# Performance work log

Hardware: AMD Instinct MI355X
Metric: run time of the kernel (lower is better)

The kernel has to match this reference:

```python
import jax, jax.numpy as jnp
import numpy as np
import math

B, S, D, H = 1, 4096, 1024, 16
HD = D // H  # head_dim = 64


def setup_inputs() -> dict:
    key = jax.random.key(0)
    ks = jax.random.split(key, 6)
    x = jax.random.normal(ks[0], (B, S, D), dtype=jnp.float32)
    # Llama-style rotary frequencies: theta = 10000^{-2i/head_dim}
    inv_freq = 1.0 / (10000.0 ** (jnp.arange(0, HD, 2, dtype=jnp.float32) / HD))  # (HD/2,)
    t = jnp.arange(S, dtype=jnp.float32)
    freqs = jnp.outer(t, inv_freq)  # (S, HD/2)
    cos = jnp.cos(freqs)
    sin = jnp.sin(freqs)
    # additive causal mask (S, S): 0 on/below diagonal, -inf above
    mask = jnp.where(jnp.tril(jnp.ones((S, S), dtype=bool)), 0.0, -jnp.inf).astype(jnp.float32)
    scale = 1.0 / math.sqrt(D)
    wq = jax.random.normal(ks[1], (D, D), dtype=jnp.float32) * scale
    wk = jax.random.normal(ks[2], (D, D), dtype=jnp.float32) * scale
    wv = jax.random.normal(ks[3], (D, D), dtype=jnp.float32) * scale
    wo = jax.random.normal(ks[4], (D, D), dtype=jnp.float32) * scale
    return {"x": x, "cos": cos, "sin": sin, "mask": mask,
            "wq": wq, "wk": wk, "wv": wv, "wo": wo, "start_pos": 0}


def _rope(t, cos, sin):
    # t: (b, s, h, hd); cos/sin: (s, hd/2). Interleaved-pair complex rotation.
    b, s, h, hd = t.shape
    tr = t.reshape(b, s, h, hd // 2, 2)
    te, to = tr[..., 0], tr[..., 1]
    c = cos[None, :, None, :]
    sn = sin[None, :, None, :]
    oe = te * c - to * sn
    oo = te * sn + to * c
    return jnp.stack([oe, oo], axis=-1).reshape(b, s, h, hd)


def reference(x, cos, sin, mask, wq, wk, wv, wo, start_pos):
    b, s, d = x.shape
    h, hd = H, HD
    # Linear layers: y = x @ W.T (torch nn.Linear convention, W is (out,in))
    xq = (x @ wq.T).reshape(b, s, h, hd)
    xk = (x @ wk.T).reshape(b, s, h, hd)
    xv = (x @ wv.T).reshape(b, s, h, hd)
    xq = _rope(xq, cos, sin)
    xk = _rope(xk, cos, sin)
    # (b, h, s, hd)
    xq = xq.transpose(0, 2, 1, 3)
    xk = xk.transpose(0, 2, 1, 3)
    xv = xv.transpose(0, 2, 1, 3)
    scores = jnp.einsum('bhqd,bhkd->bhqk', xq, xk) / math.sqrt(hd)
    scores = scores + mask[None, None, :, :]
    attn = jax.nn.softmax(scores.astype(jnp.float32), axis=-1).astype(xq.dtype)
    out = jnp.einsum('bhqk,bhkd->bhqd', attn, xv)
    out = out.transpose(0, 2, 1, 3).reshape(b, s, d)
    return out @ wo.T
```

## Files before the change

kernel.cpp:

```cpp
#include <hip/hip_runtime.h>
#include <hip/hip_bf16.h>
#include <math.h>

typedef __bf16 bf16;
typedef __bf16 bf16x4 __attribute__((ext_vector_type(4)));
typedef __bf16 bf16x8 __attribute__((ext_vector_type(8)));
typedef float floatx4 __attribute__((ext_vector_type(4)));
typedef short short4v __attribute__((ext_vector_type(4)));

#define S_LEN 4096
#define DM 1024
#define NH 16
#define HD 64

#define GM 4096
#define GN 1024
#define GK 1024
#define FST 68

#define GLDS16(gp, lp) __builtin_amdgcn_global_load_lds( \
    (const __attribute__((address_space(1))) void*)(gp), \
    (__attribute__((address_space(3))) void*)(lp), 16, 0, 0)

__global__ void cvt_bf16(const float* __restrict__ x,  const float* __restrict__ wq,
                         const float* __restrict__ wk, const float* __restrict__ wv,
                         const float* __restrict__ wo, bf16* __restrict__ dst)
{
    size_t i4 = ((size_t)blockIdx.x * 256 + threadIdx.x) * 4;
    const float* src; size_t off;
    const size_t M1 = (size_t)1 << 20;
    if      (i4 < 4 * M1) { src = x;  off = i4;          }
    else if (i4 < 5 * M1) { src = wq; off = i4 - 4 * M1; }
    else if (i4 < 6 * M1) { src = wk; off = i4 - 5 * M1; }
    else if (i4 < 7 * M1) { src = wv; off = i4 - 6 * M1; }
    else                  { src = wo; off = i4 - 7 * M1; }
    float4 v = *(const float4*)(src + off);
    bf16x4 o = { (bf16)v.x, (bf16)v.y, (bf16)v.z, (bf16)v.w };
    *(bf16x4*)(&dst[i4]) = o;
}

__launch_bounds__(256)
__global__ void gemm_qkv(const bf16* __restrict__ A,
                         const bf16* __restrict__ B0, const bf16* __restrict__ B1,
                         const bf16* __restrict__ B2,
                         const float* __restrict__ cosp, const float* __restrict__ sinp,
                         bf16* __restrict__ Qw, bf16* __restrict__ Kw,
                         bf16* __restrict__ VTw)
{
    const int bz = blockIdx.z;
    const bf16* __restrict__ B = (bz == 0) ? B0 : (bz == 1 ? B1 : B2);

    const int tid  = threadIdx.x;
    const int wave = tid >> 6;
    const int lane = tid & 63;
    const int wm   = (wave >> 1) * 32;
    const int wn   = (wave & 1) * 64;
    const int lrow = lane >> 4;
    const int lcol = lane & 15;

    const int m0 = blockIdx.y * 64;
    const int n0 = blockIdx.x * 128;

    __shared__ __align__(16) bf16 As[64 * 64];
    __shared__ __align__(16) bf16 Bs[128 * 64];

    floatx4 acc[2][4];
    #pragma unroll
    for (int i = 0; i < 2; i++)
        #pragma unroll
        for (int j = 0; j < 4; j++) acc[i][j] = (floatx4){0.f, 0.f, 0.f, 0.f};

    const bf16* ga0 = A + (size_t)(m0 + wave * 16 + (lane >> 3)) * GK + (lane & 7) * 8;
    const bf16* gb0 = B + (size_t)(n0 + wave * 32 + (lane >> 3)) * GK + (lane & 7) * 8;
    bf16* la = &As[(wave * 16) * 64];
    bf16* lb = &Bs[(wave * 32) * 64];

    for (int kt = 0; kt < GK; kt += 64) {
        #pragma unroll
        for (int i = 0; i < 2; i++)
            GLDS16(ga0 + kt + (size_t)i * 8 * GK, la + i * 8 * 64);
        #pragma unroll
        for (int i = 0; i < 4; i++)
            GLDS16(gb0 + kt + (size_t)i * 8 * GK, lb + i * 8 * 64);
        __syncthreads();
        #pragma unroll
        for (int ks = 0; ks < 2; ks++) {
            bf16x8 af[2], bfr[4];
            #pragma unroll
            for (int t = 0; t < 2; t++)
                af[t]  = *(const bf16x8*)(&As[(wm + t * 16 + lcol) * 64 + ks * 32 + lrow * 8]);
            #pragma unroll
            for (int t = 0; t < 4; t++)
                bfr[t] = *(const bf16x8*)(&Bs[(wn + t * 16 + lcol) * 64 + ks * 32 + lrow * 8]);
            #pragma unroll
            for (int mt = 0; mt < 2; mt++)
                #pragma unroll
                for (int nt = 0; nt < 4; nt++)
                    acc[mt][nt] = __builtin_amdgcn_mfma_f32_16x16x32_bf16(af[mt], bfr[nt], acc[mt][nt], 0, 0, 0);
        }
        __syncthreads();
    }

    if (bz < 2) {
        bf16* __restrict__ C = bz ? Kw : Qw;
        const bool odd = (lcol & 1);
        #pragma unroll
        for (int mt = 0; mt < 2; mt++)
            #pragma unroll
            for (int nt = 0; nt < 4; nt++) {
                int i = (nt * 16 + lcol) >> 1;
                #pragma unroll
                for (int r = 0; r < 4; r++) {
                    float v  = acc[mt][nt][r];
                    float pv = __shfl_xor(v, 1, 64);
                    int s = m0 + wm + mt * 16 + lrow * 4 + r;
                    float c  = cosp[s * 32 + i];
                    float sn = sinp[s * 32 + i];
                    float ov = odd ? (pv * sn + v * c) : (v * c - pv * sn);
                    C[(size_t)s * GN + n0 + wn + nt * 16 + lcol] = (bf16)ov;
                }
            }
    } else {
        #pragma unroll
        for (int mt = 0; mt < 2; mt++)
            #pragma unroll
            for (int nt = 0; nt < 4; nt++) {
                int col = n0 + wn + nt * 16 + lcol;
                int s   = m0 + wm + mt * 16 + lrow * 4;
                bf16x4 ov = { (bf16)acc[mt][nt][0], (bf16)acc[mt][nt][1],
                              (bf16)acc[mt][nt][2], (bf16)acc[mt][nt][3] };
                *(bf16x4*)(&VTw[(size_t)col * S_LEN + s]) = ov;
            }
    }
}

__launch_bounds__(256, 4)
__global__ void flash_attn(const bf16* __restrict__ Q, const bf16* __restrict__ K,
                           const bf16* __restrict__ VT,
                           float* __restrict__ O0, float* __restrict__ O1,
                           float* __restrict__ L0, float* __restrict__ L1)
{
    const int pi   = blockIdx.x >> 1;
    const int p    = blockIdx.x & 1;
    const int h    = blockIdx.y;
    const int tid  = threadIdx.x;
    const int wave = tid >> 6;
    const int lane = tid & 63;
    const int lrow = lane >> 4;
    const int lcol = lane & 15;

    const int qtA = pi;
    const int qtB = 63 - pi;

    float* __restrict__ Op = p ? O1 : O0;
    float* __restrict__ Lp = p ? L1 : L0;

    __shared__ __align__(16) bf16 Ks[2][64 * FST];
    __shared__ __align__(16) bf16 Vs[2][64 * FST];

    const float sc2 = 0.125f * 1.44269504088896340736f;

    const int q0A = qtA * 64 + wave * 16;
    const int q0B = qtB * 64 + wave * 16;

    const bf16* qpA = Q + (size_t)(q0A + lcol) * DM + h * HD;
    const bf16* qpB = Q + (size_t)(q0B + lcol) * DM + h * HD;
    bf16x8 qfA[2], qfB[2];
    qfA[0] = *(const bf16x8*)(qpA + 0 + lrow * 8);
    qfA[1] = *(const bf16x8*)(qpA + 32 + lrow * 8);
    qfB[0] = *(const bf16x8*)(qpB + 0 + lrow * 8);
    qfB[1] = *(const bf16x8*)(qpB + 32 + lrow * 8);

    float lA = 0.f, lB = 0.f;
    floatx4 oaccA[4], oaccB[4];
    #pragma unroll
    for (int nt = 0; nt < 4; nt++) {
        oaccA[nt] = (floatx4){0.f, 0.f, 0.f, 0.f};
        oaccB[nt] = (floatx4){0.f, 0.f, 0.f, 0.f};
    }

    const int  srow = tid >> 3;
    const int  sch  = (tid & 7) * 8;
    const bf16* kp  = K  + (size_t)srow * DM + h * HD + sch;
    const bf16* vp  = VT + (size_t)(h * HD + srow) * S_LEN + sch;
    const int  wof  = srow * FST + sch;

    {
        size_t ko = (size_t)p * 64 * DM;
        size_t vo = (size_t)p * 64;
        uint4 a = *(const uint4*)(kp + ko);
        uint4 b = *(const uint4*)(kp + ko + (size_t)32 * DM);
        uint4 c = *(const uint4*)(vp + vo);
        uint4 d = *(const uint4*)(vp + vo + (size_t)32 * S_LEN);
        *(uint4*)(&Ks[0][wof])            = a;
        *(uint4*)(&Ks[0][wof + 32 * FST]) = b;
        *(uint4*)(&Vs[0][wof])            = c;
        *(uint4*)(&Vs[0][wof + 32 * FST]) = d;
    }
    __syncthreads();

    uint4 kr0, kr1, vr0, vr1;
    for (int t = p; t <= qtB; t += 2) {
        const int  cur  = ((t - p) >> 1) & 1;
        const bool more = (t + 2 <= qtB);
        const bool actA = (t <= qtA);

        if (more) {
            size_t ko = (size_t)(t + 2) * 64 * DM;
            size_t vo = (size_t)(t + 2) * 64;
            kr0 = *(const uint4*)(kp + ko);
            kr1 = *(const uint4*)(kp + ko + (size_t)32 * DM);
            vr0 = *(const uint4*)(vp + vo);
            vr1 = *(const uint4*)(vp + vo + (size_t)32 * S_LEN);
        }

        short4v pbA[4], pbB[4];
        const bool diagA = (t == qtA);
        const bool diagB = (t == qtB);
        #pragma unroll
        for (int nt = 0; nt < 4; nt++) {
            floatx4 zB = (floatx4){0.f, 0.f, 0.f, 0.f};
            floatx4 zA = (floatx4){0.f, 0.f, 0.f, 0.f};
            #pragma unroll
            for (int ks = 0; ks < 2; ks++) {
                bf16x8 kf = *(const bf16x8*)(&Ks[cur][(nt * 16 + lcol) * FST + ks * 32 + lrow * 8]);
                zB = __builtin_amdgcn_mfma_f32_16x16x32_bf16(kf, qfB[ks], zB, 0, 0, 0);
                if (actA)
                    zA = __builtin_amdgcn_mfma_f32_16x16x32_bf16(kf, qfA[ks], zA, 0, 0, 0);
            }
            if (diagB) {
                #pragma unroll
                for (int r = 0; r < 4; r++) {
                    int kg = t * 64 + nt * 16 + lrow * 4 + r;
                    float pr = exp2f(zB[r] * sc2);
                    if (kg > q0B + lcol) pr = 0.f;
                    zB[r] = pr; lB += pr;
                }
            } else {
                #pragma unroll
                for (int r = 0; r < 4; r++) {
                    float pr = exp2f(zB[r] * sc2);
                    zB[r] = pr; lB += pr;
                }
            }
            bf16x4 pvB = { (bf16)zB[0], (bf16)zB[1], (bf16)zB[2], (bf16)zB[3] };
            pbB[nt] = __builtin_bit_cast(short4v, pvB);
            if (actA) {
                if (diagA) {
                    #pragma unroll
                    for (int r = 0; r < 4; r++) {
                        int kg = t * 64 + nt * 16 + lrow * 4 + r;
                        float pr = exp2f(zA[r] * sc2);
                        if (kg > q0A + lcol) pr = 0.f;
                        zA[r] = pr; lA += pr;
                    }
                } else {
                    #pragma unroll
                    for (int r = 0; r < 4; r++) {
                        float pr = exp2f(zA[r] * sc2);
                        zA[r] = pr; lA += pr;
                    }
                }
                bf16x4 pvA = { (bf16)zA[0], (bf16)zA[1], (bf16)zA[2], (bf16)zA[3] };
                pbA[nt] = __builtin_bit_cast(short4v, pvA);
            }
        }

        #pragma unroll
        for (int nt = 0; nt < 4; nt++)
            #pragma unroll
            for (int kt = 0; kt < 4; kt++) {
                bf16x4 va = *(const bf16x4*)(&Vs[cur][(nt * 16 + lcol) * FST + kt * 16 + lrow * 4]);
                short4v vas = __builtin_bit_cast(short4v, va);
                oaccB[nt] = __builtin_amdgcn_mfma_f32_16x16x16bf16_1k(vas, pbB[kt], oaccB[nt], 0, 0, 0);
                if (actA)
                    oaccA[nt] = __builtin_amdgcn_mfma_f32_16x16x16bf16_1k(vas, pbA[kt], oaccA[nt], 0, 0, 0);
            }

        if (more) {
            int nxt = cur ^ 1;
            *(uint4*)(&Ks[nxt][wof])            = kr0;
            *(uint4*)(&Ks[nxt][wof + 32 * FST]) = kr1;
            *(uint4*)(&Vs[nxt][wof])            = vr0;
            *(uint4*)(&Vs[nxt][wof + 32 * FST]) = vr1;
        }
        __syncthreads();
    }

    lA += __shfl_xor(lA, 16, 64);
    lA += __shfl_xor(lA, 32, 64);
    lB += __shfl_xor(lB, 16, 64);
    lB += __shfl_xor(lB, 32, 64);
    if (lrow == 0) {
        Lp[h * S_LEN + q0A + lcol] = lA;
        Lp[h * S_LEN + q0B + lcol] = lB;
    }
    #pragma unroll
    for (int nt = 0; nt < 4; nt++) {
        *(floatx4*)(&Op[(size_t)(q0A + lcol) * DM + h * HD + nt * 16 + lrow * 4]) = oaccA[nt];
        *(floatx4*)(&Op[(size_t)(q0B + lcol) * DM + h * HD + nt * 16 + lrow * 4]) = oaccB[nt];
    }
}

__global__ void combine_kernel(const float* __restrict__ O0, const float* __restrict__ O1,
                               const float* __restrict__ L0, const float* __restrict__ L1,
                               bf16* __restrict__ Aw)
{
    int i4 = (blockIdx.x * 256 + threadIdx.x) * 4;
    int q = i4 >> 10;
    int c = i4 & 1023;
    int h = c >> 6;
    float rl = 1.f / (L0[h * S_LEN + q] + L1[h * S_LEN + q]);
    float4 a = *(const float4*)(O0 + i4);
    float4 b = *(const float4*)(O1 + i4);
    bf16x4 o = { (bf16)((a.x + b.x) * rl), (bf16)((a.y + b.y) * rl),
                 (bf16)((a.z + b.z) * rl), (bf16)((a.w + b.w) * rl) };
    *(bf16x4*)(&Aw[i4]) = o;
}

__launch_bounds__(256)
__global__ void gemm_out(const bf16* __restrict__ A, const bf16* __restrict__ B,
                         float* __restrict__ out)
{
    const int tid  = threadIdx.x;
    const int wave = tid >> 6;
    const int lane = tid & 63;
    const int wm   = (wave >> 1) * 32;
    const int wn   = (wave & 1) * 64;
    const int lrow = lane >> 4;
    const int lcol = lane & 15;

    const int m0 = blockIdx.y * 64;
    const int n0 = blockIdx.x * 128;

    __shared__ __align__(16) bf16 As[64 * 64];
    __shared__ __align__(16) bf16 Bs[128 * 64];

    floatx4 acc[2][4];
    #pragma unroll
    for (int i = 0; i < 2; i++)
        #pragma unroll
        for (int j = 0; j < 4; j++) acc[i][j] = (floatx4){0.f, 0.f, 0.f, 0.f};

    const bf16* ga0 = A + (size_t)(m0 + wave * 16 + (lane >> 3)) * GK + (lane & 7) * 8;
    const bf16* gb0 = B + (size_t)(n0 + wave * 32 + (lane >> 3)) * GK + (lane & 7) * 8;
    bf16* la = &As[(wave * 16) * 64];
    bf16* lb = &Bs[(wave * 32) * 64];

    for (int kt = 0; kt < GK; kt += 64) {
        #pragma unroll
        for (int i = 0; i < 2; i++)
            GLDS16(ga0 + kt + (size_t)i * 8 * GK, la + i * 8 * 64);
        #pragma unroll
        for (int i = 0; i < 4; i++)
            GLDS16(gb0 + kt + (size_t)i * 8 * GK, lb + i * 8 * 64);
        __syncthreads();
        #pragma unroll
        for (int ks = 0; ks < 2; ks++) {
            bf16x8 af[2], bfr[4];
            #pragma unroll
            for (int t = 0; t < 2; t++)
                af[t]  = *(const bf16x8*)(&As[(wm + t * 16 + lcol) * 64 + ks * 32 + lrow * 8]);
            #pragma unroll
            for (int t = 0; t < 4; t++)
                bfr[t] = *(const bf16x8*)(&Bs[(wn + t * 16 + lcol) * 64 + ks * 32 + lrow * 8]);
            #pragma unroll
            for (int mt = 0; mt < 2; mt++)
                #pragma unroll
                for (int nt = 0; nt < 4; nt++)
                    acc[mt][nt] = __builtin_amdgcn_mfma_f32_16x16x32_bf16(af[mt], bfr[nt], acc[mt][nt], 0, 0, 0);
        }
        __syncthreads();
    }

    #pragma unroll
    for (int mt = 0; mt < 2; mt++)
        #pragma unroll
        for (int nt = 0; nt < 4; nt++)
            #pragma unroll
            for (int r = 0; r < 4; r++) {
                int row = m0 + wm + mt * 16 + lrow * 4 + r;
                int col = n0 + wn + nt * 16 + lcol;
                out[(size_t)row * GN + col] = acc[mt][nt][r];
            }
}

extern "C" void kernel_launch(void* const* d_in, const int* in_sizes, int n_in,
                              void* d_out, int out_size, void* d_ws, size_t ws_size,
                              hipStream_t stream) {
    const float* x    = (const float*)d_in[0];
    const float* cosp = (const float*)d_in[1];
    const float* sinp = (const float*)d_in[2];
    const float* wq   = (const float*)d_in[4];
    const float* wk   = (const float*)d_in[5];
    const float* wv   = (const float*)d_in[6];
    const float* wo   = (const float*)d_in[7];
    float* out = (float*)d_out;

    const size_t SD = (size_t)S_LEN * DM;
    const size_t DD = (size_t)DM * DM;
    bf16* xb  = (bf16*)d_ws;
    bf16* wqb = xb + SD;
    bf16* wkb = wqb + DD;
    bf16* wvb = wkb + DD;
    bf16* wob = wvb + DD;
    bf16* Qw  = wob + DD;
    bf16* Kw  = Qw + SD;
    bf16* VTw = Kw + SD;
    bf16* Aw  = VTw + SD;
    float* O0f = (float*)(Aw + SD);
    float* O1f = O0f + SD;
    float* L0f = O1f + SD;
    float* L1f = L0f + (size_t)S_LEN * NH;

    cvt_bf16<<<8192, 256, 0, stream>>>(x, wq, wk, wv, wo, xb);
    gemm_qkv<<<dim3(GN / 128, GM / 64, 3), 256, 0, stream>>>(
        xb, wqb, wkb, wvb, cosp, sinp, Qw, Kw, VTw);
    flash_attn<<<dim3(64, NH), 256, 0, stream>>>(Qw, Kw, VTw, O0f, O1f, L0f, L1f);
    combine_kernel<<<S_LEN * DM / 1024, 256, 0, stream>>>(O0f, O1f, L0f, L1f, Aw);
    gemm_out<<<dim3(GN / 128, GM / 64), 256, 0, stream>>>(Aw, wob, out);
}
```

Baseline: 286.9 us.

## Split attention KV range three ways, swizzle LDS tiles, add MFMA priority hints

The flash attention kernel is templated on the number of KV-range splits. It now uses three partial passes when the workspace is large enough, with a three-way combine kernel, so more blocks can fill the GPU. The padded LDS layout is replaced by an XOR-swizzled 64-wide layout, which shrinks shared memory and avoids bank conflicts. Launch bounds rise to 5 blocks per CU, s_setprio brackets the MFMA sections, and the row-sum is accumulated per register component. The cost is an extra partial-output buffer to read and write, plus possible register pressure at the higher occupancy target.

```diff
diff --git a/kernel.cpp b/kernel.cpp
--- a/kernel.cpp
+++ b/kernel.cpp
@@ -16,7 +16,6 @@
 #define GM 4096
 #define GN 1024
 #define GK 1024
-#define FST 68
 
 #define GLDS16(gp, lp) __builtin_amdgcn_global_load_lds( \
     (const __attribute__((address_space(1))) void*)(gp), \
@@ -134,29 +133,35 @@
     }
 }
 
-__launch_bounds__(256, 4)
+#define KSW(row, chunk) (((row) << 6) + ((((chunk) ^ ((row) & 7))) << 3))
+
+template<int STEP>
+__launch_bounds__(256, 5)
 __global__ void flash_attn(const bf16* __restrict__ Q, const bf16* __restrict__ K,
                            const bf16* __restrict__ VT,
                            float* __restrict__ O0, float* __restrict__ O1,
-                           float* __restrict__ L0, float* __restrict__ L1)
-{
-    const int pi   = blockIdx.x >> 1;
-    const int p    = blockIdx.x & 1;
+                           float* __restrict__ O2,
+                           float* __restrict__ L0, float* __restrict__ L1,
+                           float* __restrict__ L2)
+{
+    const int pi   = blockIdx.x / STEP;
+    const int p    = blockIdx.x % STEP;
     const int h    = blockIdx.y;
     const int tid  = threadIdx.x;
     const int wave = tid >> 6;
     const int lane = tid & 63;
     const int lrow = lane >> 4;
     const int lcol = lane & 15;
+    const int rsw  = lcol & 7;
 
     const int qtA = pi;
     const int qtB = 63 - pi;
 
-    float* __restrict__ Op = p ? O1 : O0;
-    float* __restrict__ Lp = p ? L1 : L0;
-
-    __shared__ __align__(16) bf16 Ks[2][64 * FST];
-    __shared__ __align__(16) bf16 Vs[2][64 * FST];
+    float* __restrict__ Op = (p == 0) ? O0 : (p == 1 ? O1 : O2);
+    float* __restrict__ Lp = (p == 0) ? L0 : (p == 1 ? L1 : L2);
+
+    __shared__ __align__(16) bf16 Ks[2][64 * 64];
+    __shared__ __align__(16) bf16 Vs[2][64 * 64];
 
     const float sc2 = 0.125f * 1.44269504088896340736f;
 
@@ -171,7 +176,8 @@
     qfB[0] = *(const bf16x8*)(qpB + 0 + lrow * 8);
     qfB[1] = *(const bf16x8*)(qpB + 32 + lrow * 8);
 
-    float lA = 0.f, lB = 0.f;
+    floatx4 lA4 = (floatx4){0.f, 0.f, 0.f, 0.f};
+    floatx4 lB4 = (floatx4){0.f, 0.f, 0.f, 0.f};
     floatx4 oaccA[4], oaccB[4];
     #pragma unroll
     for (int nt = 0; nt < 4; nt++) {
@@ -180,10 +186,10 @@
     }
 
     const int  srow = tid >> 3;
-    const int  sch  = (tid & 7) * 8;
-    const bf16* kp  = K  + (size_t)srow * DM + h * HD + sch;
-    const bf16* vp  = VT + (size_t)(h * HD + srow) * S_LEN + sch;
-    const int  wof  = srow * FST + sch;
+    const int  schk = tid & 7;
+    const bf16* kp  = K  + (size_t)srow * DM + h * HD + schk * 8;
+    const bf16* vp  = VT + (size_t)(h * HD + srow) * S_LEN + schk * 8;
+    const int  wof  = KSW(srow, schk);
 
     {
         size_t ko = (size_t)p * 64 * DM;
@@ -192,22 +198,22 @@
         uint4 b = *(const uint4*)(kp + ko + (size_t)32 * DM);
         uint4 c = *(const uint4*)(vp + vo);
         uint4 d = *(const uint4*)(vp + vo + (size_t)32 * S_LEN);
-        *(uint4*)(&Ks[0][wof])            = a;
-        *(uint4*)(&Ks[0][wof + 32 * FST]) = b;
-        *(uint4*)(&Vs[0][wof])            = c;
-        *(uint4*)(&Vs[0][wof + 32 * FST]) = d;
+        *(uint4*)(&Ks[0][wof])           = a;
+        *(uint4*)(&Ks[0][wof + 32 * 64]) = b;
+        *(uint4*)(&Vs[0][wof])           = c;
+        *(uint4*)(&Vs[0][wof + 32 * 64]) = d;
     }
     __syncthreads();
 
     uint4 kr0, kr1, vr0, vr1;
-    for (int t = p; t <= qtB; t += 2) {
-        const int  cur  = ((t - p) >> 1) & 1;
-        const bool more = (t + 2 <= qtB);
+    for (int t = p; t <= qtB; t += STEP) {
+        const int  cur  = ((t - p) / STEP) & 1;
+        const bool more = (t + STEP <= qtB);
         const bool actA = (t <= qtA);
 
         if (more) {
-            size_t ko = (size_t)(t + 2) * 64 * DM;
-            size_t vo = (size_t)(t + 2) * 64;
+            size_t ko = (size_t)(t + STEP) * 64 * DM;
+            size_t vo = (size_t)(t + STEP) * 64;
             kr0 = *(const uint4*)(kp + ko);
             kr1 = *(const uint4*)(kp + ko + (size_t)32 * DM);
             vr0 = *(const uint4*)(vp + vo);
@@ -221,26 +227,29 @@
         for (int nt = 0; nt < 4; nt++) {
             floatx4 zB = (floatx4){0.f, 0.f, 0.f, 0.f};
             floatx4 zA = (floatx4){0.f, 0.f, 0.f, 0.f};
+            __builtin_amdgcn_s_setprio(1);
             #pragma unroll
             for (int ks = 0; ks < 2; ks++) {
-                bf16x8 kf = *(const bf16x8*)(&Ks[cur][(nt * 16 + lcol) * FST + ks * 32 + lrow * 8]);
+                bf16x8 kf = *(const bf16x8*)(&Ks[cur][((nt * 16 + lcol) << 6) +
+                                             ((((ks << 2) + lrow) ^ rsw) << 3)]);
                 zB = __builtin_amdgcn_mfma_f32_16x16x32_bf16(kf, qfB[ks], zB, 0, 0, 0);
                 if (actA)
                     zA = __builtin_amdgcn_mfma_f32_16x16x32_bf16(kf, qfA[ks], zA, 0, 0, 0);
             }
+            __builtin_amdgcn_s_setprio(0);
             if (diagB) {
                 #pragma unroll
                 for (int r = 0; r < 4; r++) {
                     int kg = t * 64 + nt * 16 + lrow * 4 + r;
                     float pr = exp2f(zB[r] * sc2);
                     if (kg > q0B + lcol) pr = 0.f;
-                    zB[r] = pr; lB += pr;
+                    zB[r] = pr; lB4[r] += pr;
                 }
             } else {
                 #pragma unroll
                 for (int r = 0; r < 4; r++) {
                     float pr = exp2f(zB[r] * sc2);
-                    zB[r] = pr; lB += pr;
+                    zB[r] = pr; lB4[r] += pr;
                 }
             }
             bf16x4 pvB = { (bf16)zB[0], (bf16)zB[1], (bf16)zB[2], (bf16)zB[3] };
@@ -252,13 +261,13 @@
                         int kg = t * 64 + nt * 16 + lrow * 4 + r;
                         float pr = exp2f(zA[r] * sc2);
                         if (kg > q0A + lcol) pr = 0.f;
-                        zA[r] = pr; lA += pr;
+                        zA[r] = pr; lA4[r] += pr;
                     }
                 } else {
                     #pragma unroll
                     for (int r = 0; r < 4; r++) {
                         float pr = exp2f(zA[r] * sc2);
-                        zA[r] = pr; lA += pr;
+                        zA[r] = pr; lA4[r] += pr;
                     }
                 }
                 bf16x4 pvA = { (bf16)zA[0], (bf16)zA[1], (bf16)zA[2], (bf16)zA[3] };
@@ -266,27 +275,32 @@
             }
         }
 
+        __builtin_amdgcn_s_setprio(1);
         #pragma unroll
         for (int nt = 0; nt < 4; nt++)
             #pragma unroll
             for (int kt = 0; kt < 4; kt++) {
-                bf16x4 va = *(const bf16x4*)(&Vs[cur][(nt * 16 + lcol) * FST + kt * 16 + lrow * 4]);
+                bf16x4 va = *(const bf16x4*)(&Vs[cur][((nt * 16 + lcol) << 6) +
+                              ((((kt << 1) + (lrow >> 1)) ^ rsw) << 3) + ((lrow & 1) << 2)]);
                 short4v vas = __builtin_bit_cast(short4v, va);
                 oaccB[nt] = __builtin_amdgcn_mfma_f32_16x16x16bf16_1k(vas, pbB[kt], oaccB[nt], 0, 0, 0);
                 if (actA)
                     oaccA[nt] = __builtin_amdgcn_mfma_f32_16x16x16bf16_1k(vas, pbA[kt], oaccA[nt], 0, 0, 0);
             }
+        __builtin_amdgcn_s_setprio(0);
 
         if (more) {
             int nxt = cur ^ 1;
-            *(uint4*)(&Ks[nxt][wof])            = kr0;
-            *(uint4*)(&Ks[nxt][wof + 32 * FST]) = kr1;
-            *(uint4*)(&Vs[nxt][wof])            = vr0;
-            *(uint4*)(&Vs[nxt][wof + 32 * FST]) = vr1;
+            *(uint4*)(&Ks[nxt][wof])           = kr0;
+            *(uint4*)(&Ks[nxt][wof + 32 * 64]) = kr1;
+            *(uint4*)(&Vs[nxt][wof])           = vr0;
+            *(uint4*)(&Vs[nxt][wof + 32 * 64]) = vr1;
         }
         __syncthreads();
     }
 
+    float lA = lA4[0] + lA4[1] + lA4[2] + lA4[3];
+    float lB = lB4[0] + lB4[1] + lB4[2] + lB4[3];
     lA += __shfl_xor(lA, 16, 64);
     lA += __shfl_xor(lA, 32, 64);
     lB += __shfl_xor(lB, 16, 64);
@@ -302,9 +316,9 @@
     }
 }
 
-__global__ void combine_kernel(const float* __restrict__ O0, const float* __restrict__ O1,
-                               const float* __restrict__ L0, const float* __restrict__ L1,
-                               bf16* __restrict__ Aw)
+__global__ void combine2(const float* __restrict__ O0, const float* __restrict__ O1,
+                         const float* __restrict__ L0, const float* __restrict__ L1,
+                         bf16* __restrict__ Aw)
 {
     int i4 = (blockIdx.x * 256 + threadIdx.x) * 4;
     int q = i4 >> 10;
@@ -315,6 +329,25 @@
     float4 b = *(const float4*)(O1 + i4);
     bf16x4 o = { (bf16)((a.x + b.x) * rl), (bf16)((a.y + b.y) * rl),
                  (bf16)((a.z + b.z) * rl), (bf16)((a.w + b.w) * rl) };
+    *(bf16x4*)(&Aw[i4]) = o;
+}
+
+__global__ void combine3(const float* __restrict__ O0, const float* __restrict__ O1,
+                         const float* __restrict__ O2,
+                         const float* __restrict__ L0, const float* __restrict__ L1,
+                         const float* __restrict__ L2,
+                         bf16* __restrict__ Aw)
+{
+    int i4 = (blockIdx.x * 256 + threadIdx.x) * 4;
+    int q = i4 >> 10;
+    int c = i4 & 1023;
+    int h = c >> 6;
+    float rl = 1.f / (L0[h * S_LEN + q] + L1[h * S_LEN + q] + L2[h * S_LEN + q]);
+    float4 a = *(const float4*)(O0 + i4);
+    float4 b = *(const float4*)(O1 + i4);
+    float4 cc = *(const float4*)(O2 + i4);
+    bf16x4 o = { (bf16)((a.x + b.x + cc.x) * rl), (bf16)((a.y + b.y + cc.y) * rl),
+                 (bf16)((a.z + b.z + cc.z) * rl), (bf16)((a.w + b.w + cc.w) * rl) };
     *(bf16x4*)(&Aw[i4]) = o;
 }
 
@@ -412,11 +445,23 @@
     float* O1f = O0f + SD;
     float* L0f = O1f + SD;
     float* L1f = L0f + (size_t)S_LEN * NH;
+    float* O2f = L1f + (size_t)S_LEN * NH;
+    float* L2f = O2f + SD;
+    size_t need3 = (size_t)((char*)(L2f + (size_t)S_LEN * NH) - (char*)d_ws);
 
     cvt_bf16<<<8192, 256, 0, stream>>>(x, wq, wk, wv, wo, xb);
     gemm_qkv<<<dim3(GN / 128, GM / 64, 3), 256, 0, stream>>>(
         xb, wqb, wkb, wvb, cosp, sinp, Qw, Kw, VTw);
-    flash_attn<<<dim3(64, NH), 256, 0, stream>>>(Qw, Kw, VTw, O0f, O1f, L0f, L1f);
-    combine_kernel<<<S_LEN * DM / 1024, 256, 0, stream>>>(O0f, O1f, L0f, L1f, Aw);
+    if (ws_size >= need3) {
+        flash_attn<3><<<dim3(96, NH), 256, 0, stream>>>(
+            Qw, Kw, VTw, O0f, O1f, O2f, L0f, L1f, L2f);
+        combine3<<<S_LEN * DM / 1024, 256, 0, stream>>>(
+            O0f, O1f, O2f, L0f, L1f, L2f, Aw);
+    } else {
+        flash_attn<2><<<dim3(64, NH), 256, 0, stream>>>(
+            Qw, Kw, VTw, O0f, O1f, O0f, L0f, L1f, L0f);
+        combine2<<<S_LEN * DM / 1024, 256, 0, stream>>>(
+            O0f, O1f, L0f, L1f, Aw);
+    }
     gemm_out<<<dim3(GN / 128, GM / 64), 256, 0, stream>>>(Aw, wob, out);
 }
```

New measurement: 473.5 us. +65.1%, slower.

## Double-buffer and swizzle GEMM LDS tiles, fold softmax scale into Q, MFMA row sums

Applied to the files above, without the earlier changes.

Both GEMM kernels now keep two LDS buffers and prefetch the next K-tile while the current one is being computed. They also XOR-swizzle the 16-byte chunks in LDS to cut bank conflicts on the fragment reads. The attention scale times log2(e) is folded into Q in the projection epilogue, which removes a multiply per score in the softmax. The per-row softmax denominator is now accumulated with an MFMA against a ones vector instead of scalar adds and cross-lane shuffles. The costs are double the LDS per GEMM block, which can lower occupancy, and slightly different rounding because Q is scaled before the bf16 cast.

```diff
diff --git a/kernel.cpp b/kernel.cpp
--- a/kernel.cpp
+++ b/kernel.cpp
@@ -17,6 +17,8 @@
 #define GN 1024
 #define GK 1024
 #define FST 68
+
+#define QSCALE 0.18033688011112042f
 
 #define GLDS16(gp, lp) __builtin_amdgcn_global_load_lds( \
     (const __attribute__((address_space(1))) void*)(gp), \
@@ -61,8 +63,8 @@
     const int m0 = blockIdx.y * 64;
     const int n0 = blockIdx.x * 128;
 
-    __shared__ __align__(16) bf16 As[64 * 64];
-    __shared__ __align__(16) bf16 Bs[128 * 64];
+    __shared__ __align__(16) bf16 As[2][64 * 64];
+    __shared__ __align__(16) bf16 Bs[2][128 * 64];
 
     floatx4 acc[2][4];
     #pragma unroll
@@ -70,28 +72,40 @@
         #pragma unroll
         for (int j = 0; j < 4; j++) acc[i][j] = (floatx4){0.f, 0.f, 0.f, 0.f};
 
-    const bf16* ga0 = A + (size_t)(m0 + wave * 16 + (lane >> 3)) * GK + (lane & 7) * 8;
-    const bf16* gb0 = B + (size_t)(n0 + wave * 32 + (lane >> 3)) * GK + (lane & 7) * 8;
-    bf16* la = &As[(wave * 16) * 64];
-    bf16* lb = &Bs[(wave * 32) * 64];
-
+    const int swc = (((lane & 7) ^ ((lane >> 3) & 7))) * 8;
+    const bf16* ga0 = A + (size_t)(m0 + wave * 16 + (lane >> 3)) * GK + swc;
+    const bf16* gb0 = B + (size_t)(n0 + wave * 32 + (lane >> 3)) * GK + swc;
+    const int kof0 = ((0 + lrow) ^ (lcol & 7)) * 8;
+    const int kof1 = ((4 + lrow) ^ (lcol & 7)) * 8;
+
+    #pragma unroll
+    for (int i = 0; i < 2; i++)
+        GLDS16(ga0 + (size_t)i * 8 * GK, &As[0][(wave * 16 + i * 8) * 64]);
+    #pragma unroll
+    for (int i = 0; i < 4; i++)
+        GLDS16(gb0 + (size_t)i * 8 * GK, &Bs[0][(wave * 32 + i * 8) * 64]);
+    __syncthreads();
+
+    int cur = 0;
     for (int kt = 0; kt < GK; kt += 64) {
-        #pragma unroll
-        for (int i = 0; i < 2; i++)
-            GLDS16(ga0 + kt + (size_t)i * 8 * GK, la + i * 8 * 64);
-        #pragma unroll
-        for (int i = 0; i < 4; i++)
-            GLDS16(gb0 + kt + (size_t)i * 8 * GK, lb + i * 8 * 64);
-        __syncthreads();
+        if (kt + 64 < GK) {
+            #pragma unroll
+            for (int i = 0; i < 2; i++)
+                GLDS16(ga0 + kt + 64 + (size_t)i * 8 * GK, &As[cur ^ 1][(wave * 16 + i * 8) * 64]);
+            #pragma unroll
+            for (int i = 0; i < 4; i++)
+                GLDS16(gb0 + kt + 64 + (size_t)i * 8 * GK, &Bs[cur ^ 1][(wave * 32 + i * 8) * 64]);
+        }
         #pragma unroll
         for (int ks = 0; ks < 2; ks++) {
+            const int ko = ks ? kof1 : kof0;
             bf16x8 af[2], bfr[4];
             #pragma unroll
             for (int t = 0; t < 2; t++)
-                af[t]  = *(const bf16x8*)(&As[(wm + t * 16 + lcol) * 64 + ks * 32 + lrow * 8]);
+                af[t]  = *(const bf16x8*)(&As[cur][(wm + t * 16 + lcol) * 64 + ko]);
             #pragma unroll
             for (int t = 0; t < 4; t++)
-                bfr[t] = *(const bf16x8*)(&Bs[(wn + t * 16 + lcol) * 64 + ks * 32 + lrow * 8]);
+                bfr[t] = *(const bf16x8*)(&Bs[cur][(wn + t * 16 + lcol) * 64 + ko]);
             #pragma unroll
             for (int mt = 0; mt < 2; mt++)
                 #pragma unroll
@@ -99,10 +113,12 @@
                     acc[mt][nt] = __builtin_amdgcn_mfma_f32_16x16x32_bf16(af[mt], bfr[nt], acc[mt][nt], 0, 0, 0);
         }
         __syncthreads();
+        cur ^= 1;
     }
 
     if (bz < 2) {
         bf16* __restrict__ C = bz ? Kw : Qw;
+        const float qs = (bz == 0) ? QSCALE : 1.0f;
         const bool odd = (lcol & 1);
         #pragma unroll
         for (int mt = 0; mt < 2; mt++)
@@ -117,7 +133,7 @@
                     float c  = cosp[s * 32 + i];
                     float sn = sinp[s * 32 + i];
                     float ov = odd ? (pv * sn + v * c) : (v * c - pv * sn);
-                    C[(size_t)s * GN + n0 + wn + nt * 16 + lcol] = (bf16)ov;
+                    C[(size_t)s * GN + n0 + wn + nt * 16 + lcol] = (bf16)(ov * qs);
                 }
             }
     } else {
@@ -158,8 +174,6 @@
     __shared__ __align__(16) bf16 Ks[2][64 * FST];
     __shared__ __align__(16) bf16 Vs[2][64 * FST];
 
-    const float sc2 = 0.125f * 1.44269504088896340736f;
-
     const int q0A = qtA * 64 + wave * 16;
     const int q0B = qtB * 64 + wave * 16;
 
@@ -171,7 +185,12 @@
     qfB[0] = *(const bf16x8*)(qpB + 0 + lrow * 8);
     qfB[1] = *(const bf16x8*)(qpB + 32 + lrow * 8);
 
-    float lA = 0.f, lB = 0.f;
+    const bf16 one_b = (bf16)1.0f;
+    const bf16x4 onev = { one_b, one_b, one_b, one_b };
+    const short4v ones_s = __builtin_bit_cast(short4v, onev);
+
+    floatx4 laccA = (floatx4){0.f, 0.f, 0.f, 0.f};
+    floatx4 laccB = (floatx4){0.f, 0.f, 0.f, 0.f};
     floatx4 oaccA[4], oaccB[4];
     #pragma unroll
     for (int nt = 0; nt < 4; nt++) {
@@ -232,16 +251,14 @@
                 #pragma unroll
                 for (int r = 0; r < 4; r++) {
                     int kg = t * 64 + nt * 16 + lrow * 4 + r;
-                    float pr = exp2f(zB[r] * sc2);
+                    float pr = exp2f(zB[r]);
                     if (kg > q0B + lcol) pr = 0.f;
-                    zB[r] = pr; lB += pr;
+                    zB[r] = pr;
                 }
             } else {
                 #pragma unroll
-                for (int r = 0; r < 4; r++) {
-                    float pr = exp2f(zB[r] * sc2);
-                    zB[r] = pr; lB += pr;
-                }
+                for (int r = 0; r < 4; r++)
+                    zB[r] = exp2f(zB[r]);
             }
             bf16x4 pvB = { (bf16)zB[0], (bf16)zB[1], (bf16)zB[2], (bf16)zB[3] };
             pbB[nt] = __builtin_bit_cast(short4v, pvB);
@@ -250,20 +267,25 @@
                     #pragma unroll
                     for (int r = 0; r < 4; r++) {
                         int kg = t * 64 + nt * 16 + lrow * 4 + r;
-                        float pr = exp2f(zA[r] * sc2);
+                        float pr = exp2f(zA[r]);
                         if (kg > q0A + lcol) pr = 0.f;
-                        zA[r] = pr; lA += pr;
+                        zA[r] = pr;
                     }
                 } else {
                     #pragma unroll
-                    for (int r = 0; r < 4; r++) {
-                        float pr = exp2f(zA[r] * sc2);
-                        zA[r] = pr; lA += pr;
-                    }
+                    for (int r = 0; r < 4; r++)
+                        zA[r] = exp2f(zA[r]);
                 }
                 bf16x4 pvA = { (bf16)zA[0], (bf16)zA[1], (bf16)zA[2], (bf16)zA[3] };
                 pbA[nt] = __builtin_bit_cast(short4v, pvA);
             }
+        }
+
+        #pragma unroll
+        for (int kt = 0; kt < 4; kt++) {
+            laccB = __builtin_amdgcn_mfma_f32_16x16x16bf16_1k(ones_s, pbB[kt], laccB, 0, 0, 0);
+            if (actA)
+                laccA = __builtin_amdgcn_mfma_f32_16x16x16bf16_1k(ones_s, pbA[kt], laccA, 0, 0, 0);
         }
 
         #pragma unroll
@@ -287,13 +309,9 @@
         __syncthreads();
     }
 
-    lA += __shfl_xor(lA, 16, 64);
-    lA += __shfl_xor(lA, 32, 64);
-    lB += __shfl_xor(lB, 16, 64);
-    lB += __shfl_xor(lB, 32, 64);
     if (lrow == 0) {
-        Lp[h * S_LEN + q0A + lcol] = lA;
-        Lp[h * S_LEN + q0B + lcol] = lB;
+        Lp[h * S_LEN + q0A + lcol] = laccA[0];
+        Lp[h * S_LEN + q0B + lcol] = laccB[0];
     }
     #pragma unroll
     for (int nt = 0; nt < 4; nt++) {
@@ -333,8 +351,8 @@
     const int m0 = blockIdx.y * 64;
     const int n0 = blockIdx.x * 128;
 
-    __shared__ __align__(16) bf16 As[64 * 64];
-    __shared__ __align__(16) bf16 Bs[128 * 64];
+    __shared__ __align__(16) bf16 As[2][64 * 64];
+    __shared__ __align__(16) bf16 Bs[2][128 * 64];
 
     floatx4 acc[2][4];
     #pragma unroll
@@ -342,28 +360,40 @@
         #pragma unroll
         for (int j = 0; j < 4; j++) acc[i][j] = (floatx4){0.f, 0.f, 0.f, 0.f};
 
-    const bf16* ga0 = A + (size_t)(m0 + wave * 16 + (lane >> 3)) * GK + (lane & 7) * 8;
-    const bf16* gb0 = B + (size_t)(n0 + wave * 32 + (lane >> 3)) * GK + (lane & 7) * 8;
-    bf16* la = &As[(wave * 16) * 64];
-    bf16* lb = &Bs[(wave * 32) * 64];
-
+    const int swc = (((lane & 7) ^ ((lane >> 3) & 7))) * 8;
+    const bf16* ga0 = A + (size_t)(m0 + wave * 16 + (lane >> 3)) * GK + swc;
+    const bf16* gb0 = B + (size_t)(n0 + wave * 32 + (lane >> 3)) * GK + swc;
+    const int kof0 = ((0 + lrow) ^ (lcol & 7)) * 8;
+    const int kof1 = ((4 + lrow) ^ (lcol & 7)) * 8;
+
+    #pragma unroll
+    for (int i = 0; i < 2; i++)
+        GLDS16(ga0 + (size_t)i * 8 * GK, &As[0][(wave * 16 + i * 8) * 64]);
+    #pragma unroll
+    for (int i = 0; i < 4; i++)
+        GLDS16(gb0 + (size_t)i * 8 * GK, &Bs[0][(wave * 32 + i * 8) * 64]);
+    __syncthreads();
+
+    int cur = 0;
     for (int kt = 0; kt < GK; kt += 64) {
-        #pragma unroll
-        for (int i = 0; i < 2; i++)
-            GLDS16(ga0 + kt + (size_t)i * 8 * GK, la + i * 8 * 64);
-        #pragma unroll
-        for (int i = 0; i < 4; i++)
-            GLDS16(gb0 + kt + (size_t)i * 8 * GK, lb + i * 8 * 64);
-        __syncthreads();
+        if (kt + 64 < GK) {
+            #pragma unroll
+            for (int i = 0; i < 2; i++)
+                GLDS16(ga0 + kt + 64 + (size_t)i * 8 * GK, &As[cur ^ 1][(wave * 16 + i * 8) * 64]);
+            #pragma unroll
+            for (int i = 0; i < 4; i++)
+                GLDS16(gb0 + kt + 64 + (size_t)i * 8 * GK, &Bs[cur ^ 1][(wave * 32 + i * 8) * 64]);
+        }
         #pragma unroll
         for (int ks = 0; ks < 2; ks++) {
+            const int ko = ks ? kof1 : kof0;
             bf16x8 af[2], bfr[4];
             #pragma unroll
             for (int t = 0; t < 2; t++)
-                af[t]  = *(const bf16x8*)(&As[(wm + t * 16 + lcol) * 64 + ks * 32 + lrow * 8]);
+                af[t]  = *(const bf16x8*)(&As[cur][(wm + t * 16 + lcol) * 64 + ko]);
             #pragma unroll
             for (int t = 0; t < 4; t++)
-                bfr[t] = *(const bf16x8*)(&Bs[(wn + t * 16 + lcol) * 64 + ks * 32 + lrow * 8]);
+                bfr[t] = *(const bf16x8*)(&Bs[cur][(wn + t * 16 + lcol) * 64 + ko]);
             #pragma unroll
             for (int mt = 0; mt < 2; mt++)
                 #pragma unroll
@@ -371,6 +401,7 @@
                     acc[mt][nt] = __builtin_amdgcn_mfma_f32_16x16x32_bf16(af[mt], bfr[nt], acc[mt][nt], 0, 0, 0);
         }
         __syncthreads();
+        cur ^= 1;
     }
 
     #pragma unroll
```

After: 289.1 us. No clear change (+0.8%).
